# Optimization experiments

Measured on AMD Instinct MI355X. Metric: run time of the kernel, lower is better.

## Reference

```python
import jax, jax.numpy as jnp
import numpy as np


def setup_inputs() -> dict:
    key = jax.random.key(0)
    k1, k2, k3 = jax.random.split(key, 3)
    b, c, h, w = 4, 124, 64, 64
    x = jax.random.normal(k1, (b, c, h, w), dtype=jnp.float32)
    # 1x1 conv, no bias -> channel-mixing matrix [c_out, c_in]
    Wb = jax.random.normal(k2, (c, c), dtype=jnp.float32) * (1.0 / np.sqrt(c))
    gamma = jax.random.normal(k3, (1,), dtype=jnp.float32) * 0.1
    return {"x": x, "Wb": Wb, "gamma": gamma}


def reference(x, Wb, gamma):
    b, c, h, w = x.shape
    n = h * w
    xf = x.reshape(b, c, n)                      # [b, c, n]
    # NOTE: original code applies convB for B, C, and D (convC/convD unused)
    Bf = jnp.einsum('oc,bcn->bon', Wb, xf)       # [b, c, n]
    # S = softmax(B^T C, dim=last) -> [b, n, n]
    scores = jnp.einsum('bcm,bcn->bmn', Bf, Bf)
    S = jax.nn.softmax(scores, axis=2)
    # E = D @ S^T -> E[b,c,m] = sum_n D[b,c,n] * S[b,m,n]
    E = jnp.einsum('bcn,bmn->bcm', Bf, S).reshape(b, c, h, w)
    return gamma[0] * E + x
```

## Files before the change

kernel.cpp:

```cpp
#include <hip/hip_runtime.h>

typedef short short8 __attribute__((ext_vector_type(8)));
typedef short short4v __attribute__((ext_vector_type(4)));
typedef float floatx4 __attribute__((ext_vector_type(4)));

#define BB 4
#define CC 124
#define CP 128
#define NN 4096
#define NGRP 256
#define NG32 128
#define NSPLIT 4
#define KSPLIT (NN / NSPLIT)
#define TN 64
#define NCHUNK (KSPLIT / TN)

static __device__ __forceinline__ unsigned short f2bf_fast(float f) {
    return (unsigned short)((__float_as_uint(f) + 0x8000u) >> 16);
}
static __device__ __forceinline__ float bf2f(unsigned short u) {
    return __uint_as_float(((unsigned int)u) << 16);
}
static __device__ __forceinline__ unsigned int pkbf(float a, float b) {
    unsigned int ua = __float_as_uint(a) + 0x8000u;
    unsigned int ub = __float_as_uint(b) + 0x8000u;
    return __builtin_amdgcn_perm(ub, ua, 0x07060302u);
}
union PK2 { short4v s; unsigned int u[2]; };
union PK8 { short8 s; unsigned int u[4]; };

static __device__ __forceinline__ void gl16(const unsigned short* g, unsigned short* l) {
    __builtin_amdgcn_global_load_lds(
        (const __attribute__((address_space(1))) unsigned int*)g,
        (__attribute__((address_space(3))) unsigned int*)l, 16, 0, 0);
}

__global__ __launch_bounds__(256) void wtrans_kernel(const float* __restrict__ Wb,
                                                     unsigned short* __restrict__ wbt) {
    __shared__ float ws[32][125];
    const int blk = blockIdx.x;
    const int tid = threadIdx.x;
    for (int i = tid; i < 32 * CC; i += 256) {
        int ol = i / CC, c = i - ol * CC;
        int o = blk * 32 + ol;
        ws[ol][c] = (o < CC) ? Wb[o * CC + c] : 0.f;
    }
    __syncthreads();
    for (int i = tid; i < CC * 32; i += 256) {
        int c = i >> 5, ol = i & 31;
        wbt[c * CP + blk * 32 + ol] = f2bf_fast(ws[ol][c]);
    }
}

__global__ __launch_bounds__(256, 4) void bf_proj_kernel(const float* __restrict__ x,
                                                         const unsigned short* __restrict__ wbt,
                                                         unsigned short* __restrict__ kfrag,
                                                         unsigned short* __restrict__ vfrag,
                                                         float* __restrict__ m2) {
    __shared__ __align__(16) float xs[CC][36];
    __shared__ float msh[32][33];
    const int tid = threadIdx.x;
    const int b = blockIdx.y;
    const int n0 = blockIdx.x * 32;
    const float* xb = x + (size_t)b * CC * NN + n0;
    for (int i = tid; i < CC * 8; i += 256) {
        int c = i >> 3, nq = i & 7;
        *(floatx4*)&xs[c][nq * 4] = *(const floatx4*)(xb + (size_t)c * NN + nq * 4);
    }
    __syncthreads();
    const int og = tid >> 3;
    const int nidx = tid & 7;
    const int o0 = og * 4;
    float acc[4][4];
#pragma unroll
    for (int k = 0; k < 4; ++k)
#pragma unroll
        for (int j = 0; j < 4; ++j) acc[k][j] = 0.f;
    for (int c = 0; c < CC; ++c) {
        floatx4 xv = *(const floatx4*)&xs[c][nidx * 4];
        short4v wv = *(const short4v*)&wbt[c * CP + o0];
#pragma unroll
        for (int k = 0; k < 4; ++k) {
            float wf = bf2f((unsigned short)wv[k]);
            acc[k][0] += wf * xv[0];
            acc[k][1] += wf * xv[1];
            acc[k][2] += wf * xv[2];
            acc[k][3] += wf * xv[3];
        }
    }
    float sq[4] = {0.f, 0.f, 0.f, 0.f};
#pragma unroll
    for (int k = 0; k < 4; ++k)
#pragma unroll
        for (int j = 0; j < 4; ++j) sq[j] += acc[k][j] * acc[k][j];
#pragma unroll
    for (int j = 0; j < 4; ++j) msh[og][nidx * 4 + j] = sq[j];
    const int g16 = (n0 >> 4) + (nidx & 1);
    const int tK = o0 >> 5;
    const int qK = (o0 >> 3) & 3;
    const int halfo = o0 & 7;
#pragma unroll
    for (int j = 0; j < 4; ++j) {
        PK2 kv;
        kv.u[0] = pkbf(acc[0][j], acc[1][j]);
        kv.u[1] = pkbf(acc[2][j], acc[3][j]);
        int row16 = 4 * (nidx >> 1) + j;
        size_t unit = ((size_t)(b * NGRP + g16) * 4 + tK) * 64 + qK * 16 + row16;
        *(short4v*)&kfrag[unit * 8 + halfo] = kv.s;
    }
    const int g32 = n0 >> 5;
    const int quadn = nidx >> 1;
    const int halfn = (nidx & 1) * 4;
#pragma unroll
    for (int k = 0; k < 4; ++k) {
        int c = o0 + k;
        PK2 vv;
        if (c == 124) {
            vv.u[0] = 0x3f803f80u;
            vv.u[1] = 0x3f803f80u;
        } else {
            vv.u[0] = pkbf(acc[k][0], acc[k][1]);
            vv.u[1] = pkbf(acc[k][2], acc[k][3]);
        }
        size_t unit = ((size_t)(b * NG32 + g32) * 8 + (c >> 4)) * 64 + quadn * 16 + (c & 15);
        *(short4v*)&vfrag[unit * 8 + halfn] = vv.s;
    }
    __syncthreads();
    if (tid < 32) {
        float s = 0.f;
#pragma unroll
        for (int og2 = 0; og2 < 32; ++og2) s += msh[og2][tid];
        m2[(size_t)b * NN + n0 + tid] = s * 1.44269504088896340736f;
    }
}

__global__ __launch_bounds__(256, 2) void attn_kernel(const unsigned short* __restrict__ kfrag,
                                                      const unsigned short* __restrict__ vfrag,
                                                      const float* __restrict__ m2,
                                                      unsigned short* __restrict__ opart) {
    __shared__ __align__(16) unsigned short kbuf[2][16 * 512];
    __shared__ __align__(16) unsigned short vbuf[2][16 * 512];
    const int id = blockIdx.x;
    const int ghi = id & 7;
    const int r_ = id >> 3;
    const int mtile = r_ & 31;
    const int glo = r_ >> 5;
    const int grp = ghi * 2 + glo;
    const int b = grp & 3;
    const int split = grp >> 2;
    const int w = threadIdx.x >> 6;
    const int lane = threadIdx.x & 63;
    const int col = lane & 15;
    const int quad = lane >> 4;
    const int m0 = mtile * 128 + w * 32;
    const floatx4 fzero = {0.f, 0.f, 0.f, 0.f};
    const float L2E = 1.44269504088896340736f;

    short8 qf[2][4];
#pragma unroll
    for (int ms = 0; ms < 2; ++ms) {
        const int gq = (m0 >> 4) + ms;
#pragma unroll
        for (int t = 0; t < 4; ++t)
            qf[ms][t] = *(const short8*)&kfrag[((size_t)(b * NGRP + gq) * 4 + t) * 512 + lane * 8];
    }
    const int mq = 8 * (col >> 2) + (col & 3);
    float nmreg[2];
    nmreg[0] = -m2[(size_t)b * NN + m0 + mq];
    nmreg[1] = -m2[(size_t)b * NN + m0 + mq + 4];

    floatx4 oacc[2][8];
#pragma unroll
    for (int ms = 0; ms < 2; ++ms)
#pragma unroll
        for (int s8 = 0; s8 < 8; ++s8) oacc[ms][s8] = fzero;

    auto stage = [&](int ch, int sel) {
        if (w < 2) {
            const int g16b = split * (KSPLIT >> 4) + ch * 4;
#pragma unroll
            for (int i = 0; i < 8; ++i) {
                int p = w * 8 + i;
                const unsigned short* src =
                    kfrag + ((size_t)(b * NGRP + g16b + (p >> 2)) * 4 + (p & 3)) * 512 + lane * 8;
                gl16(src, &kbuf[sel][p * 512]);
            }
        } else {
            const int g32b = split * (KSPLIT >> 5) + ch * 2;
#pragma unroll
            for (int i = 0; i < 8; ++i) {
                int q = (w - 2) * 8 + i;
                const unsigned short* src =
                    vfrag + ((size_t)(b * NG32 + g32b + (q >> 3)) * 8 + (q & 7)) * 512 + lane * 8;
                gl16(src, &vbuf[sel][q * 512]);
            }
        }
    };

    stage(0, 0);
#pragma unroll 2
    for (int ch = 0; ch < NCHUNK; ++ch) {
        const int sel = ch & 1;
        __syncthreads();
        if (ch + 1 < NCHUNK) stage(ch + 1, sel ^ 1);
        floatx4 st[2][4];
#pragma unroll
        for (int ms = 0; ms < 2; ++ms)
#pragma unroll
            for (int u = 0; u < 4; ++u) st[ms][u] = fzero;
#pragma unroll
        for (int t = 0; t < 4; ++t) {
#pragma unroll
            for (int u = 0; u < 4; ++u) {
                short8 kf = *(const short8*)&kbuf[sel][((u * 4 + t) * 64 + lane) * 8];
                st[0][u] = __builtin_amdgcn_mfma_f32_16x16x32_bf16(kf, qf[0][t], st[0][u], 0, 0, 0);
                st[1][u] = __builtin_amdgcn_mfma_f32_16x16x32_bf16(kf, qf[1][t], st[1][u], 0, 0, 0);
            }
        }
        float ev[2][4][4];
#pragma unroll
        for (int ms = 0; ms < 2; ++ms)
#pragma unroll
            for (int u = 0; u < 4; ++u)
#pragma unroll
                for (int r = 0; r < 4; ++r)
                    ev[ms][u][r] = exp2f(__builtin_fmaf(st[ms][u][r], L2E, nmreg[ms]));
        PK8 af[2][2];
#pragma unroll
        for (int ms = 0; ms < 2; ++ms)
#pragma unroll
            for (int u2 = 0; u2 < 2; ++u2) {
                af[ms][u2].u[0] = pkbf(ev[ms][2 * u2][0], ev[ms][2 * u2][1]);
                af[ms][u2].u[1] = pkbf(ev[ms][2 * u2][2], ev[ms][2 * u2][3]);
                af[ms][u2].u[2] = pkbf(ev[ms][2 * u2 + 1][0], ev[ms][2 * u2 + 1][1]);
                af[ms][u2].u[3] = pkbf(ev[ms][2 * u2 + 1][2], ev[ms][2 * u2 + 1][3]);
            }
#pragma unroll
        for (int u2 = 0; u2 < 2; ++u2) {
#pragma unroll
            for (int s8 = 0; s8 < 8; ++s8) {
                short8 vf = *(const short8*)&vbuf[sel][((u2 * 8 + s8) * 64 + lane) * 8];
                oacc[0][s8] = __builtin_amdgcn_mfma_f32_16x16x32_bf16(af[0][u2].s, vf, oacc[0][s8], 0, 0, 0);
                oacc[1][s8] = __builtin_amdgcn_mfma_f32_16x16x32_bf16(af[1][u2].s, vf, oacc[1][s8], 0, 0, 0);
            }
        }
    }
    unsigned short* ob = opart + (size_t)(split * BB + b) * NN * CP;
#pragma unroll
    for (int ms = 0; ms < 2; ++ms)
#pragma unroll
        for (int s8 = 0; s8 < 8; ++s8)
#pragma unroll
            for (int r = 0; r < 4; ++r)
                ob[(size_t)(m0 + 8 * quad + 4 * ms + r) * CP + s8 * 16 + col] = f2bf_fast(oacc[ms][s8][r]);
}

__global__ __launch_bounds__(256) void combine_kernel(const unsigned short* __restrict__ opart,
                                                      const float* __restrict__ x,
                                                      const float* __restrict__ gamma,
                                                      float* __restrict__ out) {
    __shared__ float es[32 * 133];
    __shared__ float Lsh[32];
    const int t = threadIdx.x;
    const int b = blockIdx.y;
    const int m0 = blockIdx.x * 32;
    if (t < 32) {
        float L = 0.f;
#pragma unroll
        for (int s = 0; s < NSPLIT; ++s)
            L += bf2f(opart[((size_t)(s * BB + b) * NN + m0 + t) * CP + 124]);
        Lsh[t] = gamma[0] / L;
    }
    const int tc = t & 31, tm = t >> 5;
    float acc[4][4];
#pragma unroll
    for (int i = 0; i < 4; ++i)
#pragma unroll
        for (int j = 0; j < 4; ++j) acc[i][j] = 0.f;
    for (int s = 0; s < NSPLIT; ++s) {
        const unsigned short* obp = opart + ((size_t)(s * BB + b) * NN + m0 + tm * 4) * CP + tc * 4;
#pragma unroll
        for (int i = 0; i < 4; ++i) {
            short4v v = *(const short4v*)(obp + (size_t)i * CP);
            acc[i][0] += bf2f((unsigned short)v[0]);
            acc[i][1] += bf2f((unsigned short)v[1]);
            acc[i][2] += bf2f((unsigned short)v[2]);
            acc[i][3] += bf2f((unsigned short)v[3]);
        }
    }
#pragma unroll
    for (int i = 0; i < 4; ++i)
#pragma unroll
        for (int j = 0; j < 4; ++j) es[(tm * 4 + i) * 133 + tc * 4 + j] = acc[i][j];
    __syncthreads();
    const int wave = t >> 6, lane = t & 63;
    const int half = lane >> 5, lm = lane & 31;
#pragma unroll
    for (int p = 0; p < 16; ++p) {
        int c = p * 8 + wave * 2 + half;
        if (c < CC) {
            size_t base = ((size_t)b * CC + c) * NN + m0 + lm;
            out[base] = es[lm * 133 + c] * Lsh[lm] + x[base];
        }
    }
}

extern "C" void kernel_launch(void* const* d_in, const int* in_sizes, int n_in,
                              void* d_out, int out_size, void* d_ws, size_t ws_size,
                              hipStream_t stream) {
    const float* x = (const float*)d_in[0];
    const float* Wb = (const float*)d_in[1];
    const float* gamma = (const float*)d_in[2];
    float* out = (float*)d_out;

    const size_t kfrag_b = (size_t)BB * NGRP * 4 * 64 * 8 * sizeof(unsigned short);
    const size_t vfrag_b = (size_t)BB * NG32 * 8 * 64 * 8 * sizeof(unsigned short);
    const size_t m2_b = (size_t)BB * NN * sizeof(float);
    const size_t opart_b = (size_t)NSPLIT * BB * NN * CP * sizeof(unsigned short);
    const size_t wbt_b = (size_t)CC * CP * sizeof(unsigned short);
    if (ws_size < kfrag_b + vfrag_b + m2_b + opart_b + wbt_b) return;

    char* w = (char*)d_ws;
    unsigned short* kfrag = (unsigned short*)w;
    unsigned short* vfrag = (unsigned short*)(w + kfrag_b);
    float* m2 = (float*)(w + kfrag_b + vfrag_b);
    unsigned short* opart = (unsigned short*)(w + kfrag_b + vfrag_b + m2_b);
    unsigned short* wbt = (unsigned short*)(w + kfrag_b + vfrag_b + m2_b + opart_b);

    wtrans_kernel<<<dim3(4), 256, 0, stream>>>(Wb, wbt);
    bf_proj_kernel<<<dim3(NN / 32, BB), 256, 0, stream>>>(x, wbt, kfrag, vfrag, m2);
    attn_kernel<<<dim3(512), 256, 0, stream>>>(kfrag, vfrag, m2, opart);
    combine_kernel<<<dim3(NN / 32, BB), 256, 0, stream>>>(opart, x, gamma, out);
}
```

Before: 131.7 us.

## Drop LDS staging in attention, load K/V fragments directly, double split count

Removes the double-buffered global-to-LDS staging and the per-chunk block barriers in the attention kernel, so each wave reads K and V fragments straight from global memory (relying on L2/L1 reuse). The key dimension split goes from 4 to 8, doubling the grid to 1024 blocks and raising launch-bound occupancy to 4 blocks per CU. The softmax tile is processed in two halves to reduce register pressure. The projection loop gets unroll 4. Risks include redundant global traffic across the four waves, and the combine kernel now has to reduce twice as many partial outputs, assuming it reads NSPLIT.

New measurement: 227.5 us. 72.7% more time.

```diff
diff --git a/kernel.cpp b/kernel.cpp
--- a/kernel.cpp
+++ b/kernel.cpp
@@ -10,7 +10,7 @@
 #define NN 4096
 #define NGRP 256
 #define NG32 128
-#define NSPLIT 4
+#define NSPLIT 8
 #define KSPLIT (NN / NSPLIT)
 #define TN 64
 #define NCHUNK (KSPLIT / TN)
@@ -28,12 +28,6 @@
 }
 union PK2 { short4v s; unsigned int u[2]; };
 union PK8 { short8 s; unsigned int u[4]; };
-
-static __device__ __forceinline__ void gl16(const unsigned short* g, unsigned short* l) {
-    __builtin_amdgcn_global_load_lds(
-        (const __attribute__((address_space(1))) unsigned int*)g,
-        (__attribute__((address_space(3))) unsigned int*)l, 16, 0, 0);
-}
 
 __global__ __launch_bounds__(256) void wtrans_kernel(const float* __restrict__ Wb,
                                                      unsigned short* __restrict__ wbt) {
@@ -76,6 +70,7 @@
     for (int k = 0; k < 4; ++k)
 #pragma unroll
         for (int j = 0; j < 4; ++j) acc[k][j] = 0.f;
+#pragma unroll 4
     for (int c = 0; c < CC; ++c) {
         floatx4 xv = *(const floatx4*)&xs[c][nidx * 4];
         short4v wv = *(const short4v*)&wbt[c * CP + o0];
@@ -134,18 +129,16 @@
     }
 }
 
-__global__ __launch_bounds__(256, 2) void attn_kernel(const unsigned short* __restrict__ kfrag,
+__global__ __launch_bounds__(256, 4) void attn_kernel(const unsigned short* __restrict__ kfrag,
                                                       const unsigned short* __restrict__ vfrag,
                                                       const float* __restrict__ m2,
                                                       unsigned short* __restrict__ opart) {
-    __shared__ __align__(16) unsigned short kbuf[2][16 * 512];
-    __shared__ __align__(16) unsigned short vbuf[2][16 * 512];
     const int id = blockIdx.x;
     const int ghi = id & 7;
     const int r_ = id >> 3;
     const int mtile = r_ & 31;
     const int glo = r_ >> 5;
-    const int grp = ghi * 2 + glo;
+    const int grp = ghi * 4 + glo;
     const int b = grp & 3;
     const int split = grp >> 2;
     const int w = threadIdx.x >> 6;
@@ -156,13 +149,16 @@
     const floatx4 fzero = {0.f, 0.f, 0.f, 0.f};
     const float L2E = 1.44269504088896340736f;
 
+    const unsigned short* kb = kfrag + (size_t)b * NGRP * 2048;
+    const unsigned short* vb = vfrag + (size_t)b * NG32 * 4096;
+
     short8 qf[2][4];
 #pragma unroll
     for (int ms = 0; ms < 2; ++ms) {
         const int gq = (m0 >> 4) + ms;
 #pragma unroll
         for (int t = 0; t < 4; ++t)
-            qf[ms][t] = *(const short8*)&kfrag[((size_t)(b * NGRP + gq) * 4 + t) * 512 + lane * 8];
+            qf[ms][t] = *(const short8*)&kb[((size_t)gq * 4 + t) * 512 + lane * 8];
     }
     const int mq = 8 * (col >> 2) + (col & 3);
     float nmreg[2];
@@ -175,73 +171,47 @@
 #pragma unroll
         for (int s8 = 0; s8 < 8; ++s8) oacc[ms][s8] = fzero;
 
-    auto stage = [&](int ch, int sel) {
-        if (w < 2) {
-            const int g16b = split * (KSPLIT >> 4) + ch * 4;
-#pragma unroll
-            for (int i = 0; i < 8; ++i) {
-                int p = w * 8 + i;
-                const unsigned short* src =
-                    kfrag + ((size_t)(b * NGRP + g16b + (p >> 2)) * 4 + (p & 3)) * 512 + lane * 8;
-                gl16(src, &kbuf[sel][p * 512]);
-            }
-        } else {
-            const int g32b = split * (KSPLIT >> 5) + ch * 2;
-#pragma unroll
-            for (int i = 0; i < 8; ++i) {
-                int q = (w - 2) * 8 + i;
-                const unsigned short* src =
-                    vfrag + ((size_t)(b * NG32 + g32b + (q >> 3)) * 8 + (q & 7)) * 512 + lane * 8;
-                gl16(src, &vbuf[sel][q * 512]);
-            }
-        }
-    };
-
-    stage(0, 0);
 #pragma unroll 2
     for (int ch = 0; ch < NCHUNK; ++ch) {
-        const int sel = ch & 1;
-        __syncthreads();
-        if (ch + 1 < NCHUNK) stage(ch + 1, sel ^ 1);
-        floatx4 st[2][4];
-#pragma unroll
-        for (int ms = 0; ms < 2; ++ms)
-#pragma unroll
-            for (int u = 0; u < 4; ++u) st[ms][u] = fzero;
-#pragma unroll
-        for (int t = 0; t < 4; ++t) {
-#pragma unroll
-            for (int u = 0; u < 4; ++u) {
-                short8 kf = *(const short8*)&kbuf[sel][((u * 4 + t) * 64 + lane) * 8];
-                st[0][u] = __builtin_amdgcn_mfma_f32_16x16x32_bf16(kf, qf[0][t], st[0][u], 0, 0, 0);
-                st[1][u] = __builtin_amdgcn_mfma_f32_16x16x32_bf16(kf, qf[1][t], st[1][u], 0, 0, 0);
+        const int g16b = split * (KSPLIT >> 4) + ch * 4;
+        const int g32b = split * (KSPLIT >> 5) + ch * 2;
+#pragma unroll
+        for (int u2 = 0; u2 < 2; ++u2) {
+            floatx4 st[2][2];
+#pragma unroll
+            for (int ms = 0; ms < 2; ++ms)
+#pragma unroll
+                for (int u = 0; u < 2; ++u) st[ms][u] = fzero;
+#pragma unroll
+            for (int t = 0; t < 4; ++t) {
+                short8 kf0 = *(const short8*)&kb[((size_t)(g16b + 2 * u2) * 4 + t) * 512 + lane * 8];
+                short8 kf1 = *(const short8*)&kb[((size_t)(g16b + 2 * u2 + 1) * 4 + t) * 512 + lane * 8];
+                st[0][0] = __builtin_amdgcn_mfma_f32_16x16x32_bf16(kf0, qf[0][t], st[0][0], 0, 0, 0);
+                st[1][0] = __builtin_amdgcn_mfma_f32_16x16x32_bf16(kf0, qf[1][t], st[1][0], 0, 0, 0);
+                st[0][1] = __builtin_amdgcn_mfma_f32_16x16x32_bf16(kf1, qf[0][t], st[0][1], 0, 0, 0);
+                st[1][1] = __builtin_amdgcn_mfma_f32_16x16x32_bf16(kf1, qf[1][t], st[1][1], 0, 0, 0);
             }
-        }
-        float ev[2][4][4];
-#pragma unroll
-        for (int ms = 0; ms < 2; ++ms)
-#pragma unroll
-            for (int u = 0; u < 4; ++u)
-#pragma unroll
-                for (int r = 0; r < 4; ++r)
-                    ev[ms][u][r] = exp2f(__builtin_fmaf(st[ms][u][r], L2E, nmreg[ms]));
-        PK8 af[2][2];
-#pragma unroll
-        for (int ms = 0; ms < 2; ++ms)
-#pragma unroll
-            for (int u2 = 0; u2 < 2; ++u2) {
-                af[ms][u2].u[0] = pkbf(ev[ms][2 * u2][0], ev[ms][2 * u2][1]);
-                af[ms][u2].u[1] = pkbf(ev[ms][2 * u2][2], ev[ms][2 * u2][3]);
-                af[ms][u2].u[2] = pkbf(ev[ms][2 * u2 + 1][0], ev[ms][2 * u2 + 1][1]);
-                af[ms][u2].u[3] = pkbf(ev[ms][2 * u2 + 1][2], ev[ms][2 * u2 + 1][3]);
+            PK8 af[2];
+#pragma unroll
+            for (int ms = 0; ms < 2; ++ms) {
+                float e00 = exp2f(__builtin_fmaf(st[ms][0][0], L2E, nmreg[ms]));
+                float e01 = exp2f(__builtin_fmaf(st[ms][0][1], L2E, nmreg[ms]));
+                float e02 = exp2f(__builtin_fmaf(st[ms][0][2], L2E, nmreg[ms]));
+                float e03 = exp2f(__builtin_fmaf(st[ms][0][3], L2E, nmreg[ms]));
+                float e10 = exp2f(__builtin_fmaf(st[ms][1][0], L2E, nmreg[ms]));
+                float e11 = exp2f(__builtin_fmaf(st[ms][1][1], L2E, nmreg[ms]));
+                float e12 = exp2f(__builtin_fmaf(st[ms][1][2], L2E, nmreg[ms]));
+                float e13 = exp2f(__builtin_fmaf(st[ms][1][3], L2E, nmreg[ms]));
+                af[ms].u[0] = pkbf(e00, e01);
+                af[ms].u[1] = pkbf(e02, e03);
+                af[ms].u[2] = pkbf(e10, e11);
+                af[ms].u[3] = pkbf(e12, e13);
             }
 #pragma unroll
-        for (int u2 = 0; u2 < 2; ++u2) {
-#pragma unroll
             for (int s8 = 0; s8 < 8; ++s8) {
-                short8 vf = *(const short8*)&vbuf[sel][((u2 * 8 + s8) * 64 + lane) * 8];
-                oacc[0][s8] = __builtin_amdgcn_mfma_f32_16x16x32_bf16(af[0][u2].s, vf, oacc[0][s8], 0, 0, 0);
-                oacc[1][s8] = __builtin_amdgcn_mfma_f32_16x16x32_bf16(af[1][u2].s, vf, oacc[1][s8], 0, 0, 0);
+                short8 vf = *(const short8*)&vb[((size_t)(g32b + u2) * 8 + s8) * 512 + lane * 8];
+                oacc[0][s8] = __builtin_amdgcn_mfma_f32_16x16x32_bf16(af[0].s, vf, oacc[0][s8], 0, 0, 0);
+                oacc[1][s8] = __builtin_amdgcn_mfma_f32_16x16x32_bf16(af[1].s, vf, oacc[1][s8], 0, 0, 0);
             }
         }
     }
@@ -329,6 +299,6 @@
 
     wtrans_kernel<<<dim3(4), 256, 0, stream>>>(Wb, wbt);
     bf_proj_kernel<<<dim3(NN / 32, BB), 256, 0, stream>>>(x, wbt, kfrag, vfrag, m2);
-    attn_kernel<<<dim3(512), 256, 0, stream>>>(kfrag, vfrag, m2, opart);
+    attn_kernel<<<dim3(1024), 256, 0, stream>>>(kfrag, vfrag, m2, opart);
     combine_kernel<<<dim3(NN / 32, BB), 256, 0, stream>>>(opart, x, gamma, out);
 }
```

## Double attention key split, single-buffer K tiles, fold weight transpose into projection

Applied to the files above, without the earlier changes.

The key dimension is now split 8 ways instead of 4, so the attention grid doubles to 1024 blocks. The K tile is single-buffered to cut LDS use, which allows an occupancy hint of 3 blocks per CU, and K prefetch moves after the score MFMAs behind an extra barrier. The separate weight-transpose kernel is removed: each projection block now converts and transposes Wb into LDS itself. The exp computation is interleaved with bf16 packing to reduce live registers. In exchange, the partial-output buffer and the combine traffic double, each chunk pays an extra barrier, and with 1024 blocks over 3 slots per CU the grid may leave a partial last wave.

Measured after the change: 141.6 us. +7.6%, slower.

```diff
diff --git a/kernel.cpp b/kernel.cpp
--- a/kernel.cpp
+++ b/kernel.cpp
@@ -10,7 +10,7 @@
 #define NN 4096
 #define NGRP 256
 #define NG32 128
-#define NSPLIT 4
+#define NSPLIT 8
 #define KSPLIT (NN / NSPLIT)
 #define TN 64
 #define NCHUNK (KSPLIT / TN)
@@ -35,29 +35,13 @@
         (__attribute__((address_space(3))) unsigned int*)l, 16, 0, 0);
 }
 
-__global__ __launch_bounds__(256) void wtrans_kernel(const float* __restrict__ Wb,
-                                                     unsigned short* __restrict__ wbt) {
-    __shared__ float ws[32][125];
-    const int blk = blockIdx.x;
-    const int tid = threadIdx.x;
-    for (int i = tid; i < 32 * CC; i += 256) {
-        int ol = i / CC, c = i - ol * CC;
-        int o = blk * 32 + ol;
-        ws[ol][c] = (o < CC) ? Wb[o * CC + c] : 0.f;
-    }
-    __syncthreads();
-    for (int i = tid; i < CC * 32; i += 256) {
-        int c = i >> 5, ol = i & 31;
-        wbt[c * CP + blk * 32 + ol] = f2bf_fast(ws[ol][c]);
-    }
-}
-
-__global__ __launch_bounds__(256, 4) void bf_proj_kernel(const float* __restrict__ x,
-                                                         const unsigned short* __restrict__ wbt,
-                                                         unsigned short* __restrict__ kfrag,
-                                                         unsigned short* __restrict__ vfrag,
-                                                         float* __restrict__ m2) {
+__global__ __launch_bounds__(256) void bf_proj_kernel(const float* __restrict__ x,
+                                                      const float* __restrict__ Wb,
+                                                      unsigned short* __restrict__ kfrag,
+                                                      unsigned short* __restrict__ vfrag,
+                                                      float* __restrict__ m2) {
     __shared__ __align__(16) float xs[CC][36];
+    __shared__ __align__(16) unsigned short wt[CC][132];
     __shared__ float msh[32][33];
     const int tid = threadIdx.x;
     const int b = blockIdx.y;
@@ -67,6 +51,10 @@
         int c = i >> 3, nq = i & 7;
         *(floatx4*)&xs[c][nq * 4] = *(const floatx4*)(xb + (size_t)c * NN + nq * 4);
     }
+    for (int oi = tid >> 5; oi < CP; oi += 8) {
+        for (int cc = tid & 31; cc < CC; cc += 32)
+            wt[cc][oi] = (oi < CC) ? f2bf_fast(Wb[oi * CC + cc]) : (unsigned short)0;
+    }
     __syncthreads();
     const int og = tid >> 3;
     const int nidx = tid & 7;
@@ -76,9 +64,10 @@
     for (int k = 0; k < 4; ++k)
 #pragma unroll
         for (int j = 0; j < 4; ++j) acc[k][j] = 0.f;
+#pragma unroll 4
     for (int c = 0; c < CC; ++c) {
         floatx4 xv = *(const floatx4*)&xs[c][nidx * 4];
-        short4v wv = *(const short4v*)&wbt[c * CP + o0];
+        short4v wv = *(const short4v*)&wt[c][o0];
 #pragma unroll
         for (int k = 0; k < 4; ++k) {
             float wf = bf2f((unsigned short)wv[k]);
@@ -134,18 +123,18 @@
     }
 }
 
-__global__ __launch_bounds__(256, 2) void attn_kernel(const unsigned short* __restrict__ kfrag,
+__global__ __launch_bounds__(256, 3) void attn_kernel(const unsigned short* __restrict__ kfrag,
                                                       const unsigned short* __restrict__ vfrag,
                                                       const float* __restrict__ m2,
                                                       unsigned short* __restrict__ opart) {
-    __shared__ __align__(16) unsigned short kbuf[2][16 * 512];
+    __shared__ __align__(16) unsigned short kbuf[16 * 512];
     __shared__ __align__(16) unsigned short vbuf[2][16 * 512];
     const int id = blockIdx.x;
     const int ghi = id & 7;
     const int r_ = id >> 3;
     const int mtile = r_ & 31;
     const int glo = r_ >> 5;
-    const int grp = ghi * 2 + glo;
+    const int grp = ghi * 4 + glo;
     const int b = grp & 3;
     const int split = grp >> 2;
     const int w = threadIdx.x >> 6;
@@ -156,13 +145,16 @@
     const floatx4 fzero = {0.f, 0.f, 0.f, 0.f};
     const float L2E = 1.44269504088896340736f;
 
+    const unsigned short* kb = kfrag + (size_t)b * NGRP * 2048;
+    const unsigned short* vb = vfrag + (size_t)b * NG32 * 4096;
+
     short8 qf[2][4];
 #pragma unroll
     for (int ms = 0; ms < 2; ++ms) {
         const int gq = (m0 >> 4) + ms;
 #pragma unroll
         for (int t = 0; t < 4; ++t)
-            qf[ms][t] = *(const short8*)&kfrag[((size_t)(b * NGRP + gq) * 4 + t) * 512 + lane * 8];
+            qf[ms][t] = *(const short8*)&kb[((size_t)gq * 4 + t) * 512 + lane * 8];
     }
     const int mq = 8 * (col >> 2) + (col & 3);
     float nmreg[2];
@@ -175,34 +167,33 @@
 #pragma unroll
         for (int s8 = 0; s8 < 8; ++s8) oacc[ms][s8] = fzero;
 
-    auto stage = [&](int ch, int sel) {
-        if (w < 2) {
-            const int g16b = split * (KSPLIT >> 4) + ch * 4;
-#pragma unroll
-            for (int i = 0; i < 8; ++i) {
-                int p = w * 8 + i;
-                const unsigned short* src =
-                    kfrag + ((size_t)(b * NGRP + g16b + (p >> 2)) * 4 + (p & 3)) * 512 + lane * 8;
-                gl16(src, &kbuf[sel][p * 512]);
-            }
-        } else {
-            const int g32b = split * (KSPLIT >> 5) + ch * 2;
-#pragma unroll
-            for (int i = 0; i < 8; ++i) {
-                int q = (w - 2) * 8 + i;
-                const unsigned short* src =
-                    vfrag + ((size_t)(b * NG32 + g32b + (q >> 3)) * 8 + (q & 7)) * 512 + lane * 8;
-                gl16(src, &vbuf[sel][q * 512]);
-            }
+    auto stageK = [&](int ch) {
+        const int g16b = split * (KSPLIT >> 4) + ch * 4;
+#pragma unroll
+        for (int i = 0; i < 4; ++i) {
+            int p = w * 4 + i;
+            const unsigned short* src =
+                kb + ((size_t)(g16b + (p >> 2)) * 4 + (p & 3)) * 512 + lane * 8;
+            gl16(src, &kbuf[p * 512]);
         }
     };
-
-    stage(0, 0);
-#pragma unroll 2
+    auto stageV = [&](int ch, int sel) {
+        const int g32b = split * (KSPLIT >> 5) + ch * 2;
+#pragma unroll
+        for (int i = 0; i < 4; ++i) {
+            int q = w * 4 + i;
+            const unsigned short* src =
+                vb + ((size_t)(g32b + (q >> 3)) * 8 + (q & 7)) * 512 + lane * 8;
+            gl16(src, &vbuf[sel][q * 512]);
+        }
+    };
+
+    stageK(0);
+    stageV(0, 0);
     for (int ch = 0; ch < NCHUNK; ++ch) {
         const int sel = ch & 1;
         __syncthreads();
-        if (ch + 1 < NCHUNK) stage(ch + 1, sel ^ 1);
+        if (ch + 1 < NCHUNK) stageV(ch + 1, sel ^ 1);
         floatx4 st[2][4];
 #pragma unroll
         for (int ms = 0; ms < 2; ++ms)
@@ -212,29 +203,32 @@
         for (int t = 0; t < 4; ++t) {
 #pragma unroll
             for (int u = 0; u < 4; ++u) {
-                short8 kf = *(const short8*)&kbuf[sel][((u * 4 + t) * 64 + lane) * 8];
+                short8 kf = *(const short8*)&kbuf[((u * 4 + t) * 64 + lane) * 8];
                 st[0][u] = __builtin_amdgcn_mfma_f32_16x16x32_bf16(kf, qf[0][t], st[0][u], 0, 0, 0);
                 st[1][u] = __builtin_amdgcn_mfma_f32_16x16x32_bf16(kf, qf[1][t], st[1][u], 0, 0, 0);
             }
         }
-        float ev[2][4][4];
-#pragma unroll
-        for (int ms = 0; ms < 2; ++ms)
-#pragma unroll
-            for (int u = 0; u < 4; ++u)
-#pragma unroll
-                for (int r = 0; r < 4; ++r)
-                    ev[ms][u][r] = exp2f(__builtin_fmaf(st[ms][u][r], L2E, nmreg[ms]));
+        __syncthreads();
+        if (ch + 1 < NCHUNK) stageK(ch + 1);
         PK8 af[2][2];
 #pragma unroll
-        for (int ms = 0; ms < 2; ++ms)
+        for (int ms = 0; ms < 2; ++ms) {
 #pragma unroll
             for (int u2 = 0; u2 < 2; ++u2) {
-                af[ms][u2].u[0] = pkbf(ev[ms][2 * u2][0], ev[ms][2 * u2][1]);
-                af[ms][u2].u[1] = pkbf(ev[ms][2 * u2][2], ev[ms][2 * u2][3]);
-                af[ms][u2].u[2] = pkbf(ev[ms][2 * u2 + 1][0], ev[ms][2 * u2 + 1][1]);
-                af[ms][u2].u[3] = pkbf(ev[ms][2 * u2 + 1][2], ev[ms][2 * u2 + 1][3]);
+                float e00 = exp2f(__builtin_fmaf(st[ms][2 * u2][0], L2E, nmreg[ms]));
+                float e01 = exp2f(__builtin_fmaf(st[ms][2 * u2][1], L2E, nmreg[ms]));
+                float e02 = exp2f(__builtin_fmaf(st[ms][2 * u2][2], L2E, nmreg[ms]));
+                float e03 = exp2f(__builtin_fmaf(st[ms][2 * u2][3], L2E, nmreg[ms]));
+                float e10 = exp2f(__builtin_fmaf(st[ms][2 * u2 + 1][0], L2E, nmreg[ms]));
+                float e11 = exp2f(__builtin_fmaf(st[ms][2 * u2 + 1][1], L2E, nmreg[ms]));
+                float e12 = exp2f(__builtin_fmaf(st[ms][2 * u2 + 1][2], L2E, nmreg[ms]));
+                float e13 = exp2f(__builtin_fmaf(st[ms][2 * u2 + 1][3], L2E, nmreg[ms]));
+                af[ms][u2].u[0] = pkbf(e00, e01);
+                af[ms][u2].u[1] = pkbf(e02, e03);
+                af[ms][u2].u[2] = pkbf(e10, e11);
+                af[ms][u2].u[3] = pkbf(e12, e13);
             }
+        }
 #pragma unroll
         for (int u2 = 0; u2 < 2; ++u2) {
 #pragma unroll
@@ -317,18 +311,15 @@
     const size_t vfrag_b = (size_t)BB * NG32 * 8 * 64 * 8 * sizeof(unsigned short);
     const size_t m2_b = (size_t)BB * NN * sizeof(float);
     const size_t opart_b = (size_t)NSPLIT * BB * NN * CP * sizeof(unsigned short);
-    const size_t wbt_b = (size_t)CC * CP * sizeof(unsigned short);
-    if (ws_size < kfrag_b + vfrag_b + m2_b + opart_b + wbt_b) return;
+    if (ws_size < kfrag_b + vfrag_b + m2_b + opart_b) return;
 
     char* w = (char*)d_ws;
     unsigned short* kfrag = (unsigned short*)w;
     unsigned short* vfrag = (unsigned short*)(w + kfrag_b);
     float* m2 = (float*)(w + kfrag_b + vfrag_b);
     unsigned short* opart = (unsigned short*)(w + kfrag_b + vfrag_b + m2_b);
-    unsigned short* wbt = (unsigned short*)(w + kfrag_b + vfrag_b + m2_b + opart_b);
-
-    wtrans_kernel<<<dim3(4), 256, 0, stream>>>(Wb, wbt);
-    bf_proj_kernel<<<dim3(NN / 32, BB), 256, 0, stream>>>(x, wbt, kfrag, vfrag, m2);
-    attn_kernel<<<dim3(512), 256, 0, stream>>>(kfrag, vfrag, m2, opart);
+
+    bf_proj_kernel<<<dim3(NN / 32, BB), 256, 0, stream>>>(x, Wb, kfrag, vfrag, m2);
+    attn_kernel<<<dim3(1024), 256, 0, stream>>>(kfrag, vfrag, m2, opart);
     combine_kernel<<<dim3(NN / 32, BB), 256, 0, stream>>>(opart, x, gamma, out);
 }
```

## Software-pipeline QK^T and softmax-PV across chunks with triple-buffered V

Applied to the files above, without the earlier changes.

Restructures the attention loop so each iteration computes S for chunk ch while doing exp and P·V for chunk ch-1. V gets a third shared-memory buffer so the previous chunk's V stays valid while the next one is staged. The aim is to overlap MFMA score work with exp/pack work and hide dependency latency. It costs more LDS (which may lower occupancy at 2 blocks per CU) and more registers for the carried scores; it also adds an unroll pragma on the projection loop.

New measurement: 133.5 us. No clear change (+1.4%).

```diff
diff --git a/kernel.cpp b/kernel.cpp
--- a/kernel.cpp
+++ b/kernel.cpp
@@ -76,6 +76,7 @@
     for (int k = 0; k < 4; ++k)
 #pragma unroll
         for (int j = 0; j < 4; ++j) acc[k][j] = 0.f;
+#pragma unroll 4
     for (int c = 0; c < CC; ++c) {
         floatx4 xv = *(const floatx4*)&xs[c][nidx * 4];
         short4v wv = *(const short4v*)&wbt[c * CP + o0];
@@ -139,7 +140,7 @@
                                                       const float* __restrict__ m2,
                                                       unsigned short* __restrict__ opart) {
     __shared__ __align__(16) unsigned short kbuf[2][16 * 512];
-    __shared__ __align__(16) unsigned short vbuf[2][16 * 512];
+    __shared__ __align__(16) unsigned short vbuf[3][16 * 512];
     const int id = blockIdx.x;
     const int ghi = id & 7;
     const int r_ = id >> 3;
@@ -156,13 +157,16 @@
     const floatx4 fzero = {0.f, 0.f, 0.f, 0.f};
     const float L2E = 1.44269504088896340736f;
 
+    const unsigned short* kb = kfrag + (size_t)b * NGRP * 2048;
+    const unsigned short* vb = vfrag + (size_t)b * NG32 * 4096;
+
     short8 qf[2][4];
 #pragma unroll
     for (int ms = 0; ms < 2; ++ms) {
         const int gq = (m0 >> 4) + ms;
 #pragma unroll
         for (int t = 0; t < 4; ++t)
-            qf[ms][t] = *(const short8*)&kfrag[((size_t)(b * NGRP + gq) * 4 + t) * 512 + lane * 8];
+            qf[ms][t] = *(const short8*)&kb[((size_t)gq * 4 + t) * 512 + lane * 8];
     }
     const int mq = 8 * (col >> 2) + (col & 3);
     float nmreg[2];
@@ -175,34 +179,69 @@
 #pragma unroll
         for (int s8 = 0; s8 < 8; ++s8) oacc[ms][s8] = fzero;
 
-    auto stage = [&](int ch, int sel) {
+    auto stage = [&](int ch) {
         if (w < 2) {
+            const int selK = ch & 1;
             const int g16b = split * (KSPLIT >> 4) + ch * 4;
 #pragma unroll
             for (int i = 0; i < 8; ++i) {
                 int p = w * 8 + i;
                 const unsigned short* src =
-                    kfrag + ((size_t)(b * NGRP + g16b + (p >> 2)) * 4 + (p & 3)) * 512 + lane * 8;
-                gl16(src, &kbuf[sel][p * 512]);
+                    kb + ((size_t)(g16b + (p >> 2)) * 4 + (p & 3)) * 512 + lane * 8;
+                gl16(src, &kbuf[selK][p * 512]);
             }
         } else {
+            const int selV = ch % 3;
             const int g32b = split * (KSPLIT >> 5) + ch * 2;
 #pragma unroll
             for (int i = 0; i < 8; ++i) {
                 int q = (w - 2) * 8 + i;
                 const unsigned short* src =
-                    vfrag + ((size_t)(b * NG32 + g32b + (q >> 3)) * 8 + (q & 7)) * 512 + lane * 8;
-                gl16(src, &vbuf[sel][q * 512]);
+                    vb + ((size_t)(g32b + (q >> 3)) * 8 + (q & 7)) * 512 + lane * 8;
+                gl16(src, &vbuf[selV][q * 512]);
             }
         }
     };
 
-    stage(0, 0);
+    auto softmax_pv = [&](floatx4 stp[2][4], int cp) {
+        const int selVp = cp % 3;
+        PK8 af[2][2];
+#pragma unroll
+        for (int ms = 0; ms < 2; ++ms) {
+#pragma unroll
+            for (int u2 = 0; u2 < 2; ++u2) {
+                float e00 = exp2f(__builtin_fmaf(stp[ms][2 * u2][0], L2E, nmreg[ms]));
+                float e01 = exp2f(__builtin_fmaf(stp[ms][2 * u2][1], L2E, nmreg[ms]));
+                float e02 = exp2f(__builtin_fmaf(stp[ms][2 * u2][2], L2E, nmreg[ms]));
+                float e03 = exp2f(__builtin_fmaf(stp[ms][2 * u2][3], L2E, nmreg[ms]));
+                float e10 = exp2f(__builtin_fmaf(stp[ms][2 * u2 + 1][0], L2E, nmreg[ms]));
+                float e11 = exp2f(__builtin_fmaf(stp[ms][2 * u2 + 1][1], L2E, nmreg[ms]));
+                float e12 = exp2f(__builtin_fmaf(stp[ms][2 * u2 + 1][2], L2E, nmreg[ms]));
+                float e13 = exp2f(__builtin_fmaf(stp[ms][2 * u2 + 1][3], L2E, nmreg[ms]));
+                af[ms][u2].u[0] = pkbf(e00, e01);
+                af[ms][u2].u[1] = pkbf(e02, e03);
+                af[ms][u2].u[2] = pkbf(e10, e11);
+                af[ms][u2].u[3] = pkbf(e12, e13);
+            }
+        }
+#pragma unroll
+        for (int u2 = 0; u2 < 2; ++u2) {
+#pragma unroll
+            for (int s8 = 0; s8 < 8; ++s8) {
+                short8 vf = *(const short8*)&vbuf[selVp][((u2 * 8 + s8) * 64 + lane) * 8];
+                oacc[0][s8] = __builtin_amdgcn_mfma_f32_16x16x32_bf16(af[0][u2].s, vf, oacc[0][s8], 0, 0, 0);
+                oacc[1][s8] = __builtin_amdgcn_mfma_f32_16x16x32_bf16(af[1][u2].s, vf, oacc[1][s8], 0, 0, 0);
+            }
+        }
+    };
+
+    stage(0);
+    floatx4 stp[2][4];
 #pragma unroll 2
     for (int ch = 0; ch < NCHUNK; ++ch) {
-        const int sel = ch & 1;
+        const int selK = ch & 1;
         __syncthreads();
-        if (ch + 1 < NCHUNK) stage(ch + 1, sel ^ 1);
+        if (ch + 1 < NCHUNK) stage(ch + 1);
         floatx4 st[2][4];
 #pragma unroll
         for (int ms = 0; ms < 2; ++ms)
@@ -212,39 +251,19 @@
         for (int t = 0; t < 4; ++t) {
 #pragma unroll
             for (int u = 0; u < 4; ++u) {
-                short8 kf = *(const short8*)&kbuf[sel][((u * 4 + t) * 64 + lane) * 8];
+                short8 kf = *(const short8*)&kbuf[selK][((u * 4 + t) * 64 + lane) * 8];
                 st[0][u] = __builtin_amdgcn_mfma_f32_16x16x32_bf16(kf, qf[0][t], st[0][u], 0, 0, 0);
                 st[1][u] = __builtin_amdgcn_mfma_f32_16x16x32_bf16(kf, qf[1][t], st[1][u], 0, 0, 0);
             }
         }
-        float ev[2][4][4];
+        if (ch > 0) softmax_pv(stp, ch - 1);
 #pragma unroll
         for (int ms = 0; ms < 2; ++ms)
 #pragma unroll
-            for (int u = 0; u < 4; ++u)
-#pragma unroll
-                for (int r = 0; r < 4; ++r)
-                    ev[ms][u][r] = exp2f(__builtin_fmaf(st[ms][u][r], L2E, nmreg[ms]));
-        PK8 af[2][2];
-#pragma unroll
-        for (int ms = 0; ms < 2; ++ms)
-#pragma unroll
-            for (int u2 = 0; u2 < 2; ++u2) {
-                af[ms][u2].u[0] = pkbf(ev[ms][2 * u2][0], ev[ms][2 * u2][1]);
-                af[ms][u2].u[1] = pkbf(ev[ms][2 * u2][2], ev[ms][2 * u2][3]);
-                af[ms][u2].u[2] = pkbf(ev[ms][2 * u2 + 1][0], ev[ms][2 * u2 + 1][1]);
-                af[ms][u2].u[3] = pkbf(ev[ms][2 * u2 + 1][2], ev[ms][2 * u2 + 1][3]);
-            }
-#pragma unroll
-        for (int u2 = 0; u2 < 2; ++u2) {
-#pragma unroll
-            for (int s8 = 0; s8 < 8; ++s8) {
-                short8 vf = *(const short8*)&vbuf[sel][((u2 * 8 + s8) * 64 + lane) * 8];
-                oacc[0][s8] = __builtin_amdgcn_mfma_f32_16x16x32_bf16(af[0][u2].s, vf, oacc[0][s8], 0, 0, 0);
-                oacc[1][s8] = __builtin_amdgcn_mfma_f32_16x16x32_bf16(af[1][u2].s, vf, oacc[1][s8], 0, 0, 0);
-            }
-        }
-    }
+            for (int u = 0; u < 4; ++u) stp[ms][u] = st[ms][u];
+    }
+    softmax_pv(stp, NCHUNK - 1);
+
     unsigned short* ob = opart + (size_t)(split * BB + b) * NN * CP;
 #pragma unroll
     for (int ms = 0; ms < 2; ++ms)
```
